# Kernel tuning notes

Hardware: AMD Instinct MI355X
Metric: run time of the kernel (lower is better)

Reference implementation:

```python
import jax, jax.numpy as jnp
import numpy as np

B, N, NPOINT, NSAMPLE = 16, 4096, 1024, 32
RADIUS = 0.4
MLP = [64, 64, 128]
IN_CH = 6
EPS = 1e-5


def setup_inputs() -> dict:
    key = jax.random.key(0)
    ks = jax.random.split(key, 2 + 2 * len(MLP))
    inp = {
        "xyz": jax.random.normal(ks[0], (B, 3, N), jnp.float32),
        "points": jax.random.normal(ks[1], (B, 3, N), jnp.float32),
    }
    c_in = IN_CH
    for i, c_out in enumerate(MLP):
        inp[f"W{i}"] = jax.random.normal(ks[2 + 2 * i], (c_out, c_in), jnp.float32) / np.sqrt(c_in).astype(np.float32)
        inp[f"b{i}"] = jnp.zeros((c_out,), jnp.float32)
        inp[f"g{i}"] = jnp.ones((c_out,), jnp.float32)
        inp[f"beta{i}"] = jnp.zeros((c_out,), jnp.float32)
        c_in = c_out
    return inp


def _gather(points, idx):
    # points: [B, N, C], idx: [B, ...] int -> [B, ..., C]
    Bv = points.shape[0]
    flat = idx.reshape(Bv, -1)
    out = jnp.take_along_axis(points, flat[..., None], axis=1)
    return out.reshape(idx.shape + (points.shape[-1],))


def _fps(xyz, npoint):
    # xyz: [B, N, 3] -> centroid indices [B, npoint]
    Bv, Nv, _ = xyz.shape
    bidx = jnp.arange(Bv)

    def step(carry, _):
        dist, far = carry
        cen = xyz[bidx, far][:, None, :]                 # [B,1,3]
        d = jnp.sum((xyz - cen) ** 2, axis=-1)           # [B,N]
        dist = jnp.minimum(dist, d)
        return (dist, jnp.argmax(dist, axis=-1)), far

    init = (jnp.full((Bv, Nv), 1e10, xyz.dtype), jnp.zeros((Bv,), jnp.int32))
    _, cents = jax.lax.scan(step, init, None, length=npoint)
    return jnp.transpose(cents)                          # [B, npoint]


def _square_distance(src, dst):
    # src [B,S,3], dst [B,N,3] -> [B,S,N]
    return (jnp.sum(src ** 2, -1)[:, :, None]
            + jnp.sum(dst ** 2, -1)[:, None, :]
            - 2.0 * jnp.einsum('bsc,bnc->bsn', src, dst))


def _ball_query(radius, nsample, xyz, new_xyz):
    Nv = xyz.shape[1]
    sqr = _square_distance(new_xyz, xyz)                 # [B,S,N]
    arange = jnp.arange(Nv, dtype=jnp.int32)[None, None, :]
    idx = jnp.where(sqr > radius ** 2, Nv, arange)       # invalid -> sentinel N
    idx = jnp.sort(idx, axis=-1)[:, :, :nsample]         # [B,S,K]
    first = idx[:, :, :1]
    return jnp.where(idx == Nv, first, idx)


def reference(xyz, points, W0, b0, g0, beta0, W1, b1, g1, beta1, W2, b2, g2, beta2):
    xyz_t = jnp.transpose(xyz, (0, 2, 1))                # [B,N,3]
    pts_t = jnp.transpose(points, (0, 2, 1))             # [B,N,D]

    fps_idx = _fps(xyz_t, NPOINT)                        # [B,S]
    new_xyz = _gather(xyz_t, fps_idx)                    # [B,S,3]
    idx = _ball_query(RADIUS, NSAMPLE, xyz_t, new_xyz)   # [B,S,K]

    g_xyz = _gather(xyz_t, idx) - new_xyz[:, :, None, :] # [B,S,K,3]
    g_pts = _gather(pts_t, idx)                          # [B,S,K,D]
    feats = jnp.concatenate([g_xyz, g_pts], axis=-1)     # [B,S,K,C]

    for W, b, g, be in ((W0, b0, g0, beta0), (W1, b1, g1, beta1), (W2, b2, g2, beta2)):
        feats = jnp.einsum('bskc,oc->bsko', feats, W) + b
        mean = feats.mean(axis=(0, 1, 2))                # BN train mode stats
        var = feats.var(axis=(0, 1, 2))
        feats = g * (feats - mean) * jax.lax.rsqrt(var + EPS) + be
        feats = jax.nn.relu(feats)

    out = feats.max(axis=2)                              # max over nsample -> [B,S,C]
    return jnp.transpose(new_xyz, (0, 2, 1)), jnp.transpose(out, (0, 2, 1))
```

## Files before the change

### kernel.cpp

```cpp
#include <hip/hip_runtime.h>
#include <hip/hip_bf16.h>

#define B_ 16
#define N_ 4096
#define S_ 1024
#define K_ 32
#define R_ (B_*S_*K_)
#define NBLK_ (R_/64)

typedef unsigned short u16;
typedef __attribute__((ext_vector_type(8))) short bf16x8;
typedef __attribute__((ext_vector_type(4))) float f32x4;

__device__ __forceinline__ u16 f2bf(float f) {
    __hip_bfloat16 h = __float2bfloat16(f);
    return __builtin_bit_cast(u16, h);
}
__device__ __forceinline__ float bf2f(u16 u) {
    unsigned x = ((unsigned)u) << 16;
    return __builtin_bit_cast(float, x);
}

template <int CTRL>
__device__ __forceinline__ double dpp_max_f64(double v) {
    unsigned long long b = (unsigned long long)__double_as_longlong(v);
    int lo = (int)(unsigned)b;
    int hi = (int)(unsigned)(b >> 32);
    int olo = __builtin_amdgcn_update_dpp(lo, lo, CTRL, 0xF, 0xF, false);
    int ohi = __builtin_amdgcn_update_dpp(hi, hi, CTRL, 0xF, 0xF, false);
    double o = __longlong_as_double(
        (long long)(((unsigned long long)(unsigned)ohi << 32) | (unsigned)olo));
    return fmax(v, o);
}

__device__ __forceinline__ double packd(double d, int idx) {
    unsigned long long b = (unsigned long long)__double_as_longlong(d);
    b = (b & ~0xFFFull) | (unsigned)idx;
    return __longlong_as_double((long long)b);
}

__global__ __launch_bounds__(512, 1) void fps_kernel(const float* __restrict__ xyz,
                                                     float* __restrict__ out0) {
    const int b = blockIdx.x;
    const int tid = threadIdx.x;
    const int lane = tid & 63, wid = tid >> 6;
    __shared__ double4 cd[N_];
    __shared__ double candd[2][8];
    const float* xb = xyz + (size_t)b * 3 * N_;

    double x64[8], y64[8], z64[8], q64[8], dist[8];
#pragma unroll
    for (int j = 0; j < 8; ++j) {
        int i = tid + j * 512;
        float x = xb[i], y = xb[N_ + i], z = xb[2 * N_ + i];
        double dx = (double)x, dy = (double)y, dz = (double)z;
        double q = dx * dx + dy * dy + dz * dz;
        double4 v; v.x = -2.0 * dx; v.y = -2.0 * dy; v.z = -2.0 * dz; v.w = q + 1.0;
        cd[i] = v;
        x64[j] = dx; y64[j] = dy; z64[j] = dz; q64[j] = q;
        dist[j] = 1e30;
    }
    __syncthreads();

    int far = 0;
    int f0 = 0, f1 = 0;
    for (int s = 0; s < 1023; ++s) {
        double4 C = cd[far];
        f0 = (tid == s) ? far : f0;
        f1 = (tid + 512 == s) ? far : f1;
#pragma unroll
        for (int j = 0; j < 8; ++j) {
            double d = fma(C.x, x64[j], fma(C.y, y64[j], fma(C.z, z64[j], q64[j] + C.w)));
            dist[j] = fmin(dist[j], packd(d, tid | (j << 9)));
        }
        double k = fmax(fmax(fmax(dist[0], dist[1]), fmax(dist[2], dist[3])),
                        fmax(fmax(dist[4], dist[5]), fmax(dist[6], dist[7])));
        k = dpp_max_f64<0x111>(k);
        k = dpp_max_f64<0x112>(k);
        k = dpp_max_f64<0x114>(k);
        k = dpp_max_f64<0x118>(k);
        k = dpp_max_f64<0x142>(k);
        k = dpp_max_f64<0x143>(k);
        int buf = s & 1;
        if (lane == 63) candd[buf][wid] = k;
        __syncthreads();
        double k2 = candd[buf][lane & 7];
        k2 = dpp_max_f64<0xB1>(k2);
        k2 = dpp_max_f64<0x4E>(k2);
        k2 = dpp_max_f64<0x124>(k2);
        unsigned lo = (unsigned)(unsigned long long)__double_as_longlong(k2);
        far = (int)(__builtin_amdgcn_readfirstlane(lo) & 0xFFFu);
    }
    if (tid == 511) f1 = far;
    {
        double4 c0 = cd[f0];
        out0[(size_t)b * 3072 + tid]        = (float)(-0.5 * c0.x);
        out0[(size_t)b * 3072 + 1024 + tid] = (float)(-0.5 * c0.y);
        out0[(size_t)b * 3072 + 2048 + tid] = (float)(-0.5 * c0.z);
        double4 c1 = cd[f1];
        out0[(size_t)b * 3072 + 512 + tid]        = (float)(-0.5 * c1.x);
        out0[(size_t)b * 3072 + 1024 + 512 + tid] = (float)(-0.5 * c1.y);
        out0[(size_t)b * 3072 + 2048 + 512 + tid] = (float)(-0.5 * c1.z);
    }
}

__global__ __launch_bounds__(256) void prep_kernel(const float* __restrict__ xyz,
                                                   const float* __restrict__ W1,
                                                   const float* __restrict__ W2,
                                                   u16* __restrict__ W1bf,
                                                   u16* __restrict__ W2bf,
                                                   double4* __restrict__ xyzq) {
    int t = blockIdx.x * 256 + threadIdx.x;
    if (t < 4096) W1bf[t] = f2bf(W1[t]);
    if (t < 8192) W2bf[t] = f2bf(W2[t]);
    int b = t >> 12, i = t & 4095;
    const float* xb = xyz + (size_t)b * 3 * N_;
    double x = (double)xb[i], y = (double)xb[N_ + i], z = (double)xb[2 * N_ + i];
    double4 v; v.x = x; v.y = y; v.z = z; v.w = x * x + y * y + z * z;
    xyzq[t] = v;
}

__global__ __launch_bounds__(256) void ballq_gather(
        const double4* __restrict__ xyzq, const float* __restrict__ out0,
        const float* __restrict__ xyz, const float* __restrict__ pts,
        int* __restrict__ idxbuf, float* __restrict__ F,
        float* __restrict__ part0) {
    __shared__ int idxs[4][32];
    __shared__ float Ftile[128][6];
    __shared__ float red[8][27];
    int wid = threadIdx.x >> 6, lane = threadIdx.x & 63;
    int m = blockIdx.x * 4 + wid;
    int b = m >> 10, s = m & 1023;
    const double4* pb = xyzq + (size_t)b * N_;
    double cx = (double)out0[b * 3072 + s];
    double cy = (double)out0[b * 3072 + 1024 + s];
    double cz = (double)out0[b * 3072 + 2048 + s];
    double c2 = cx * cx + cy * cy + cz * cz;
    const double rr = 0.4 * 0.4;
    int* ob = idxbuf + (size_t)m * K_;
    int cnt = 0, first = -1;
    for (int ch = 0; ch < N_ / 64; ++ch) {
        int i = ch * 64 + lane;
        double4 p = pb[i];
        double dot = cx * p.x + cy * p.y + cz * p.z;
        double sqr = (c2 + p.w) - 2.0 * dot;
        bool in = !(sqr > rr);
        unsigned long long mask = __ballot(in);
        if (in) {
            int pos = cnt + __popcll(mask & ((1ull << lane) - 1ull));
            if (pos < K_) { ob[pos] = i; idxs[wid][pos] = i; }
        }
        if (cnt == 0 && mask) first = ch * 64 + (__ffsll((long long)mask) - 1);
        cnt += __popcll(mask);
        if (cnt >= K_) break;
    }
    if (cnt < K_ && lane >= cnt && lane < K_) { ob[lane] = first; idxs[wid][lane] = first; }
    __syncthreads();
    if (lane < 32) {
        int i = idxs[wid][lane];
        int rl = wid * 32 + lane;
        long rw = (long)m * 32 + lane;
        float cxf = out0[b * 3072 + s], cyf = out0[b * 3072 + 1024 + s], czf = out0[b * 3072 + 2048 + s];
        const float* xb = xyz + (size_t)b * 3 * N_;
        const float* pp = pts + (size_t)b * 3 * N_;
        float f0v = xb[i] - cxf, f1v = xb[N_ + i] - cyf, f2v = xb[2 * N_ + i] - czf;
        float f3v = pp[i], f4v = pp[N_ + i], f5v = pp[2 * N_ + i];
        Ftile[rl][0] = f0v; Ftile[rl][1] = f1v; Ftile[rl][2] = f2v;
        Ftile[rl][3] = f3v; Ftile[rl][4] = f4v; Ftile[rl][5] = f5v;
        float* Fg = F + rw * 6;
        Fg[0] = f0v; Fg[1] = f1v; Fg[2] = f2v; Fg[3] = f3v; Fg[4] = f4v; Fg[5] = f5v;
    }
    __syncthreads();
    int t = threadIdx.x;
    if (t < 216) {
        const int c1t[27] = {0,1,2,3,4,5, 0,0,0,0,0,0, 1,1,1,1,1, 2,2,2,2, 3,3,3, 4,4, 5};
        const int c2t[27] = {0,1,2,3,4,5, 0,1,2,3,4,5, 1,2,3,4,5, 2,3,4,5, 3,4,5, 4,5, 5};
        int st = t % 27, g = t / 27;
        float acc = 0.f;
        if (st < 6) {
            for (int r = g * 16; r < g * 16 + 16; ++r) acc += Ftile[r][st];
        } else {
            int a = c1t[st], c = c2t[st];
            for (int r = g * 16; r < g * 16 + 16; ++r) acc += Ftile[r][a] * Ftile[r][c];
        }
        red[g][st] = acc;
    }
    __syncthreads();
    if (t < 27) {
        float a = 0.f;
#pragma unroll
        for (int g = 0; g < 8; ++g) a += red[g][t];
        part0[(size_t)blockIdx.x * 27 + t] = a;
    }
}

__global__ __launch_bounds__(256) void reduce27(const float* __restrict__ part0,
                                                double* __restrict__ G) {
    int st = blockIdx.x;
    int tid = threadIdx.x;
    double s = 0.0;
    for (int i = tid; i < 4096; i += 256) s += (double)part0[(size_t)i * 27 + st];
    __shared__ double ss[256];
    ss[tid] = s;
    __syncthreads();
    for (int m = 128; m > 0; m >>= 1) {
        if (tid < m) ss[tid] += ss[tid + m];
        __syncthreads();
    }
    if (tid == 0) G[st] = ss[0];
}

__global__ __launch_bounds__(64) void stats0_final(const double* __restrict__ G,
                                                   const float* __restrict__ W0,
                                                   const float* __restrict__ b0,
                                                   const float* __restrict__ g0,
                                                   const float* __restrict__ beta0,
                                                   float* __restrict__ scale0,
                                                   float* __restrict__ shift0) {
    int o = threadIdx.x;
    double w[6], mvec[6];
#pragma unroll
    for (int c = 0; c < 6; ++c) { w[c] = (double)W0[o * 6 + c]; mvec[c] = G[c]; }
    double dot = 0.0;
#pragma unroll
    for (int c = 0; c < 6; ++c) dot += w[c] * mvec[c];
    const double Rd = (double)R_;
    double bb = (double)b0[o];
    double mu = dot / Rd + bb;
    double quad = 0.0;
    int k = 6;
#pragma unroll
    for (int a = 0; a < 6; ++a)
#pragma unroll
        for (int c = a; c < 6; ++c) {
            double g = G[k++];
            quad += (a == c) ? w[a] * w[c] * g : 2.0 * w[a] * w[c] * g;
        }
    double ey2 = (quad + 2.0 * bb * dot) / Rd + bb * bb;
    double var = ey2 - mu * mu;
    double sc = (double)g0[o] / sqrt(var + 1e-5);
    scale0[o] = (float)sc;
    shift0[o] = (float)((double)beta0[o] - mu * sc);
}

__global__ __launch_bounds__(256) void reduce_stats(const float2* __restrict__ part,
                                                    int nblk, int C,
                                                    const float* __restrict__ g,
                                                    const float* __restrict__ beta,
                                                    float* __restrict__ scale,
                                                    float* __restrict__ shift) {
    int o = blockIdx.x;
    int tid = threadIdx.x;
    double s = 0.0, q = 0.0;
    for (int i = tid; i < nblk; i += 256) {
        float2 v = part[(size_t)i * C + o];
        s += (double)v.x; q += (double)v.y;
    }
    __shared__ double ss[256], qq[256];
    ss[tid] = s; qq[tid] = q;
    __syncthreads();
    for (int m = 128; m > 0; m >>= 1) {
        if (tid < m) { ss[tid] += ss[tid + m]; qq[tid] += qq[tid + m]; }
        __syncthreads();
    }
    if (tid == 0) {
        const double Rd = (double)R_;
        double mean = ss[0] / Rd;
        double var = qq[0] / Rd - mean * mean;
        double sc = (double)g[o] / sqrt(var + 1e-5);
        scale[o] = (float)sc;
        shift[o] = (float)((double)beta[o] - mean * sc);
    }
}

__global__ __launch_bounds__(256) void layer1_mfma(
        const float* __restrict__ F, const float* __restrict__ W0,
        const float* __restrict__ b0, const float* __restrict__ scale0,
        const float* __restrict__ shift0, const u16* __restrict__ W1bf,
        const float* __restrict__ b1, u16* __restrict__ Y1bf,
        float2* __restrict__ part) {
    __shared__ float Fs[64][6];
    __shared__ float W0s[384];
    __shared__ float b0s[64], sc0[64], sh0[64];
    __shared__ u16 Xs[64][72];
    __shared__ float ssum[16][64];
    __shared__ float ssq[16][64];
    int tid = threadIdx.x;
    long rowbase = (long)blockIdx.x * 64;
    for (int t = tid; t < 384; t += 256) { Fs[t / 6][t % 6] = F[rowbase * 6 + t]; W0s[t] = W0[t]; }
    if (tid < 64) { b0s[tid] = b0[tid]; sc0[tid] = scale0[tid]; sh0[tid] = shift0[tid]; }
    __syncthreads();
    {
        int o = tid & 63, rg = tid >> 6;
        float w[6];
#pragma unroll
        for (int c = 0; c < 6; ++c) w[c] = W0s[o * 6 + c];
        float sc = sc0[o], sh = sh0[o], bb = b0s[o];
#pragma unroll
        for (int rr = 0; rr < 16; ++rr) {
            int rl = rg * 16 + rr;
            float y = bb;
#pragma unroll
            for (int c = 0; c < 6; ++c) y += Fs[rl][c] * w[c];
            Xs[rl][o] = f2bf(fmaxf(sc * y + sh, 0.f));
        }
    }
    __syncthreads();
    int l = tid & 63, w = tid >> 6;
    int ar = l & 15, kg = l >> 4;
    bf16x8 a0 = *(const bf16x8*)&Xs[w * 16 + ar][kg * 8];
    bf16x8 a1 = *(const bf16x8*)&Xs[w * 16 + ar][32 + kg * 8];
    f32x4 acc[4];
#pragma unroll
    for (int t4 = 0; t4 < 4; ++t4) acc[t4] = (f32x4){0.f, 0.f, 0.f, 0.f};
#pragma unroll
    for (int t4 = 0; t4 < 4; ++t4) {
        const u16* wp = &W1bf[(t4 * 16 + ar) * 64 + kg * 8];
        bf16x8 bfr0 = *(const bf16x8*)wp;
        bf16x8 bfr1 = *(const bf16x8*)(wp + 32);
        acc[t4] = __builtin_amdgcn_mfma_f32_16x16x32_bf16(a0, bfr0, acc[t4], 0, 0, 0);
        acc[t4] = __builtin_amdgcn_mfma_f32_16x16x32_bf16(a1, bfr1, acc[t4], 0, 0, 0);
    }
#pragma unroll
    for (int t4 = 0; t4 < 4; ++t4) {
        int col = t4 * 16 + ar;
        float bb = b1[col];
        float s = 0.f, q = 0.f;
#pragma unroll
        for (int r = 0; r < 4; ++r) {
            float y = acc[t4][r] + bb;
            int row = w * 16 + kg * 4 + r;
            Y1bf[(rowbase + row) * 64 + col] = f2bf(y);
            s += y; q += y * y;
        }
        ssum[w * 4 + kg][col] = s;
        ssq[w * 4 + kg][col] = q;
    }
    __syncthreads();
    if (tid < 64) {
        float s = 0.f, q = 0.f;
#pragma unroll
        for (int i = 0; i < 16; ++i) { s += ssum[i][tid]; q += ssq[i][tid]; }
        part[(size_t)blockIdx.x * 64 + tid] = make_float2(s, q);
    }
}

__global__ __launch_bounds__(256) void layer2_mfma(
        const u16* __restrict__ Y1bf, const float* __restrict__ scale1,
        const float* __restrict__ shift1, const u16* __restrict__ W2bf,
        const float* __restrict__ b2, float* __restrict__ gmax,
        float* __restrict__ gmin, float2* __restrict__ part) {
    __shared__ u16 Xs[64][72];
    __shared__ float sc1s[64], sh1s[64];
    __shared__ float mxs[16][128], mns[16][128];
    __shared__ float ssum[16][128], ssq[16][128];
    int tid = threadIdx.x;
    long rowbase = (long)blockIdx.x * 64;
    if (tid < 64) { sc1s[tid] = scale1[tid]; sh1s[tid] = shift1[tid]; }
    __syncthreads();
    {
        int r = tid >> 2, seg = (tid & 3) * 16;
        const u16* yp = &Y1bf[(rowbase + r) * 64 + seg];
        bf16x8 v0 = *(const bf16x8*)yp;
        bf16x8 v1 = *(const bf16x8*)(yp + 8);
#pragma unroll
        for (int j = 0; j < 8; ++j) {
            float x0 = fmaxf(sc1s[seg + j] * bf2f((u16)v0[j]) + sh1s[seg + j], 0.f);
            float x1 = fmaxf(sc1s[seg + 8 + j] * bf2f((u16)v1[j]) + sh1s[seg + 8 + j], 0.f);
            Xs[r][seg + j] = f2bf(x0);
            Xs[r][seg + 8 + j] = f2bf(x1);
        }
    }
    __syncthreads();
    int l = tid & 63, w = tid >> 6;
    int ar = l & 15, kg = l >> 4;
    bf16x8 a0 = *(const bf16x8*)&Xs[w * 16 + ar][kg * 8];
    bf16x8 a1 = *(const bf16x8*)&Xs[w * 16 + ar][32 + kg * 8];
    f32x4 acc[8];
#pragma unroll
    for (int t8 = 0; t8 < 8; ++t8) acc[t8] = (f32x4){0.f, 0.f, 0.f, 0.f};
#pragma unroll
    for (int t8 = 0; t8 < 8; ++t8) {
        const u16* wp = &W2bf[(t8 * 16 + ar) * 64 + kg * 8];
        bf16x8 bfr0 = *(const bf16x8*)wp;
        bf16x8 bfr1 = *(const bf16x8*)(wp + 32);
        acc[t8] = __builtin_amdgcn_mfma_f32_16x16x32_bf16(a0, bfr0, acc[t8], 0, 0, 0);
        acc[t8] = __builtin_amdgcn_mfma_f32_16x16x32_bf16(a1, bfr1, acc[t8], 0, 0, 0);
    }
#pragma unroll
    for (int t8 = 0; t8 < 8; ++t8) {
        int col = t8 * 16 + ar;
        float bb = b2[col];
        float y0 = acc[t8][0] + bb, y1 = acc[t8][1] + bb;
        float y2 = acc[t8][2] + bb, y3 = acc[t8][3] + bb;
        ssum[w * 4 + kg][col] = y0 + y1 + y2 + y3;
        ssq[w * 4 + kg][col] = y0 * y0 + y1 * y1 + y2 * y2 + y3 * y3;
        mxs[w * 4 + kg][col] = fmaxf(fmaxf(y0, y1), fmaxf(y2, y3));
        mns[w * 4 + kg][col] = fminf(fminf(y0, y1), fminf(y2, y3));
    }
    __syncthreads();
    if (tid < 128) {
        int col = tid;
        float s = 0.f, q = 0.f;
        float m0 = -3.0e38f, m1 = -3.0e38f, n0 = 3.0e38f, n1 = 3.0e38f;
#pragma unroll
        for (int i = 0; i < 8; ++i) {
            s += ssum[i][col]; q += ssq[i][col];
            m0 = fmaxf(m0, mxs[i][col]); n0 = fminf(n0, mns[i][col]);
        }
#pragma unroll
        for (int i = 8; i < 16; ++i) {
            s += ssum[i][col]; q += ssq[i][col];
            m1 = fmaxf(m1, mxs[i][col]); n1 = fminf(n1, mns[i][col]);
        }
        part[(size_t)blockIdx.x * 128 + col] = make_float2(s, q);
        gmax[((size_t)blockIdx.x * 2 + 0) * 128 + col] = m0;
        gmax[((size_t)blockIdx.x * 2 + 1) * 128 + col] = m1;
        gmin[((size_t)blockIdx.x * 2 + 0) * 128 + col] = n0;
        gmin[((size_t)blockIdx.x * 2 + 1) * 128 + col] = n1;
    }
}

__global__ __launch_bounds__(256) void final_kernel(const float* __restrict__ gmax,
                                                    const float* __restrict__ gmin,
                                                    const float* __restrict__ scale2,
                                                    const float* __restrict__ shift2,
                                                    float* __restrict__ out1) {
    int b = blockIdx.x, st = blockIdx.y, ot = blockIdx.z;
    __shared__ float tile[32][33];
    int tid = threadIdx.x;
    for (int e = tid; e < 1024; e += 256) {
        int sl = e >> 5, ol = e & 31;
        int s = st * 32 + sl, o = ot * 32 + ol;
        size_t m = (size_t)b * 1024 + s;
        float sc = scale2[o];
        float v = (sc >= 0.f) ? gmax[m * 128 + o] : gmin[m * 128 + o];
        tile[sl][ol] = fmaxf(sc * v + shift2[o], 0.f);
    }
    __syncthreads();
    for (int e = tid; e < 1024; e += 256) {
        int ol = e >> 5, sl = e & 31;
        int s = st * 32 + sl, o = ot * 32 + ol;
        out1[(size_t)b * 131072 + (size_t)o * 1024 + s] = tile[sl][ol];
    }
}

extern "C" void kernel_launch(void* const* d_in, const int* in_sizes, int n_in,
                              void* d_out, int out_size, void* d_ws, size_t ws_size,
                              hipStream_t stream) {
    const float* xyz   = (const float*)d_in[0];
    const float* pts   = (const float*)d_in[1];
    const float* W0    = (const float*)d_in[2];
    const float* b0    = (const float*)d_in[3];
    const float* g0    = (const float*)d_in[4];
    const float* beta0 = (const float*)d_in[5];
    const float* W1    = (const float*)d_in[6];
    const float* b1    = (const float*)d_in[7];
    const float* g1    = (const float*)d_in[8];
    const float* beta1 = (const float*)d_in[9];
    const float* W2    = (const float*)d_in[10];
    const float* b2    = (const float*)d_in[11];
    const float* g2    = (const float*)d_in[12];
    const float* beta2 = (const float*)d_in[13];

    float* out0 = (float*)d_out;
    float* out1 = (float*)d_out + 49152;

    char* w = (char*)d_ws;
    size_t off = 0;
    double4* xyzq = (double4*)(w + off);  off += (size_t)B_ * N_ * 32;
    int*    idxbuf = (int*)(w + off);    off += (size_t)R_ * 4;
    float*  F      = (float*)(w + off);  off += (size_t)R_ * 6 * 4;
    u16*    Y1bf   = (u16*)(w + off);    off += (size_t)R_ * 64 * 2;
    float*  gmax   = (float*)(w + off);  off += (size_t)B_ * S_ * 128 * 4;
    float*  gmin   = (float*)(w + off);  off += (size_t)B_ * S_ * 128 * 4;
    float2* part   = (float2*)(w + off); off += (size_t)NBLK_ * 128 * 2 * 4;
    float*  part0  = (float*)(w + off);  off += (size_t)4096 * 27 * 4;
    double* G27    = (double*)(w + off); off += 32 * 8;
    u16*    W1bf   = (u16*)(w + off);    off += 4096 * 2;
    u16*    W2bf   = (u16*)(w + off);    off += 8192 * 2;
    float*  ss     = (float*)(w + off);  off += 512 * 4;
    float* scale0 = ss,       *shift0 = ss + 64;
    float* scale1 = ss + 128, *shift1 = ss + 192;
    float* scale2 = ss + 256, *shift2 = ss + 384;

    prep_kernel<<<256, 256, 0, stream>>>(xyz, W1, W2, W1bf, W2bf, xyzq);
    fps_kernel<<<B_, 512, 0, stream>>>(xyz, out0);
    ballq_gather<<<(B_ * S_) / 4, 256, 0, stream>>>(xyzq, out0, xyz, pts, idxbuf, F, part0);
    reduce27<<<27, 256, 0, stream>>>(part0, G27);
    stats0_final<<<1, 64, 0, stream>>>(G27, W0, b0, g0, beta0, scale0, shift0);
    layer1_mfma<<<NBLK_, 256, 0, stream>>>(F, W0, b0, scale0, shift0, W1bf, b1, Y1bf, part);
    reduce_stats<<<64, 256, 0, stream>>>(part, NBLK_, 64, g1, beta1, scale1, shift1);
    layer2_mfma<<<NBLK_, 256, 0, stream>>>(Y1bf, scale1, shift1, W2bf, b2, gmax, gmin, part);
    reduce_stats<<<128, 256, 0, stream>>>(part, NBLK_, 128, g2, beta2, scale2, shift2);
    final_kernel<<<dim3(B_, 32, 4), 256, 0, stream>>>(gmax, gmin, scale2, shift2, out1);
}
```

Measured before the change: 813.7 us.

## Double MLP block tiles to 128 rows and share one LDS reduction buffer

The layer1 and layer2 MFMA kernels now handle 128 rows per block with 512 threads, which halves the number of per-block partial-stat records for reduce_stats. Layer2 replaces its four separate LDS reduction arrays with one buffer that is reused in sequence for sum, sum of squares, max and min, so shared memory stays small at the larger tile. The price is more barriers and recomputing bias-added values. The gather in ballq_gather also spreads the xyz and points loads across all 64 lanes instead of 32.

```diff
diff --git a/kernel.cpp b/kernel.cpp
--- a/kernel.cpp
+++ b/kernel.cpp
@@ -6,7 +6,7 @@
 #define S_ 1024
 #define K_ 32
 #define R_ (B_*S_*K_)
-#define NBLK_ (R_/64)
+#define NB1_ (R_/128)
 
 typedef unsigned short u16;
 typedef __attribute__((ext_vector_type(8))) short bf16x8;
@@ -156,19 +156,25 @@
     }
     if (cnt < K_ && lane >= cnt && lane < K_) { ob[lane] = first; idxs[wid][lane] = first; }
     __syncthreads();
-    if (lane < 32) {
-        int i = idxs[wid][lane];
-        int rl = wid * 32 + lane;
-        long rw = (long)m * 32 + lane;
-        float cxf = out0[b * 3072 + s], cyf = out0[b * 3072 + 1024 + s], czf = out0[b * 3072 + 2048 + s];
-        const float* xb = xyz + (size_t)b * 3 * N_;
-        const float* pp = pts + (size_t)b * 3 * N_;
-        float f0v = xb[i] - cxf, f1v = xb[N_ + i] - cyf, f2v = xb[2 * N_ + i] - czf;
-        float f3v = pp[i], f4v = pp[N_ + i], f5v = pp[2 * N_ + i];
-        Ftile[rl][0] = f0v; Ftile[rl][1] = f1v; Ftile[rl][2] = f2v;
-        Ftile[rl][3] = f3v; Ftile[rl][4] = f4v; Ftile[rl][5] = f5v;
+    {
+        int l2 = lane & 31;
+        int i = idxs[wid][l2];
+        int rl = wid * 32 + l2;
+        long rw = (long)m * 32 + l2;
         float* Fg = F + rw * 6;
-        Fg[0] = f0v; Fg[1] = f1v; Fg[2] = f2v; Fg[3] = f3v; Fg[4] = f4v; Fg[5] = f5v;
+        if (lane < 32) {
+            float cxf = out0[b * 3072 + s], cyf = out0[b * 3072 + 1024 + s],
+                  czf = out0[b * 3072 + 2048 + s];
+            const float* xb = xyz + (size_t)b * 3 * N_;
+            float f0v = xb[i] - cxf, f1v = xb[N_ + i] - cyf, f2v = xb[2 * N_ + i] - czf;
+            Ftile[rl][0] = f0v; Ftile[rl][1] = f1v; Ftile[rl][2] = f2v;
+            Fg[0] = f0v; Fg[1] = f1v; Fg[2] = f2v;
+        } else {
+            const float* pp = pts + (size_t)b * 3 * N_;
+            float f3v = pp[i], f4v = pp[N_ + i], f5v = pp[2 * N_ + i];
+            Ftile[rl][3] = f3v; Ftile[rl][4] = f4v; Ftile[rl][5] = f5v;
+            Fg[3] = f3v; Fg[4] = f4v; Fg[5] = f5v;
+        }
     }
     __syncthreads();
     int t = threadIdx.x;
@@ -273,21 +279,22 @@
     }
 }
 
-__global__ __launch_bounds__(256) void layer1_mfma(
+__global__ __launch_bounds__(512) void layer1_mfma(
         const float* __restrict__ F, const float* __restrict__ W0,
         const float* __restrict__ b0, const float* __restrict__ scale0,
         const float* __restrict__ shift0, const u16* __restrict__ W1bf,
         const float* __restrict__ b1, u16* __restrict__ Y1bf,
         float2* __restrict__ part) {
-    __shared__ float Fs[64][6];
+    __shared__ float Fs[128][6];
     __shared__ float W0s[384];
     __shared__ float b0s[64], sc0[64], sh0[64];
-    __shared__ u16 Xs[64][72];
-    __shared__ float ssum[16][64];
-    __shared__ float ssq[16][64];
+    __shared__ u16 Xs[128][72];
+    __shared__ float ssum[32][64];
+    __shared__ float ssq[32][64];
     int tid = threadIdx.x;
-    long rowbase = (long)blockIdx.x * 64;
-    for (int t = tid; t < 384; t += 256) { Fs[t / 6][t % 6] = F[rowbase * 6 + t]; W0s[t] = W0[t]; }
+    long rowbase = (long)blockIdx.x * 128;
+    for (int t = tid; t < 768; t += 512) Fs[t / 6][t % 6] = F[rowbase * 6 + t];
+    if (tid < 384) W0s[tid] = W0[tid];
     if (tid < 64) { b0s[tid] = b0[tid]; sc0[tid] = scale0[tid]; sh0[tid] = shift0[tid]; }
     __syncthreads();
     {
@@ -340,22 +347,21 @@
     if (tid < 64) {
         float s = 0.f, q = 0.f;
 #pragma unroll
-        for (int i = 0; i < 16; ++i) { s += ssum[i][tid]; q += ssq[i][tid]; }
+        for (int i = 0; i < 32; ++i) { s += ssum[i][tid]; q += ssq[i][tid]; }
         part[(size_t)blockIdx.x * 64 + tid] = make_float2(s, q);
     }
 }
 
-__global__ __launch_bounds__(256) void layer2_mfma(
+__global__ __launch_bounds__(512) void layer2_mfma(
         const u16* __restrict__ Y1bf, const float* __restrict__ scale1,
         const float* __restrict__ shift1, const u16* __restrict__ W2bf,
         const float* __restrict__ b2, float* __restrict__ gmax,
         float* __restrict__ gmin, float2* __restrict__ part) {
-    __shared__ u16 Xs[64][72];
+    __shared__ u16 Xs[128][72];
     __shared__ float sc1s[64], sh1s[64];
-    __shared__ float mxs[16][128], mns[16][128];
-    __shared__ float ssum[16][128], ssq[16][128];
+    __shared__ float red[32][128];
     int tid = threadIdx.x;
-    long rowbase = (long)blockIdx.x * 64;
+    long rowbase = (long)blockIdx.x * 128;
     if (tid < 64) { sc1s[tid] = scale1[tid]; sh1s[tid] = shift1[tid]; }
     __syncthreads();
     {
@@ -387,37 +393,58 @@
         acc[t8] = __builtin_amdgcn_mfma_f32_16x16x32_bf16(a0, bfr0, acc[t8], 0, 0, 0);
         acc[t8] = __builtin_amdgcn_mfma_f32_16x16x32_bf16(a1, bfr1, acc[t8], 0, 0, 0);
     }
+    float ybias[8];
+#pragma unroll
+    for (int t8 = 0; t8 < 8; ++t8) ybias[t8] = b2[t8 * 16 + ar];
 #pragma unroll
     for (int t8 = 0; t8 < 8; ++t8) {
-        int col = t8 * 16 + ar;
-        float bb = b2[col];
-        float y0 = acc[t8][0] + bb, y1 = acc[t8][1] + bb;
-        float y2 = acc[t8][2] + bb, y3 = acc[t8][3] + bb;
-        ssum[w * 4 + kg][col] = y0 + y1 + y2 + y3;
-        ssq[w * 4 + kg][col] = y0 * y0 + y1 * y1 + y2 * y2 + y3 * y3;
-        mxs[w * 4 + kg][col] = fmaxf(fmaxf(y0, y1), fmaxf(y2, y3));
-        mns[w * 4 + kg][col] = fminf(fminf(y0, y1), fminf(y2, y3));
+        float y0 = acc[t8][0] + ybias[t8], y1 = acc[t8][1] + ybias[t8];
+        float y2 = acc[t8][2] + ybias[t8], y3 = acc[t8][3] + ybias[t8];
+        red[w * 4 + kg][t8 * 16 + ar] = y0 + y1 + y2 + y3;
+    }
+    __syncthreads();
+    float psum = 0.f;
+    if (tid < 128) { for (int i = 0; i < 32; ++i) psum += red[i][tid]; }
+    __syncthreads();
+#pragma unroll
+    for (int t8 = 0; t8 < 8; ++t8) {
+        float y0 = acc[t8][0] + ybias[t8], y1 = acc[t8][1] + ybias[t8];
+        float y2 = acc[t8][2] + ybias[t8], y3 = acc[t8][3] + ybias[t8];
+        red[w * 4 + kg][t8 * 16 + ar] = y0 * y0 + y1 * y1 + y2 * y2 + y3 * y3;
     }
     __syncthreads();
     if (tid < 128) {
-        int col = tid;
-        float s = 0.f, q = 0.f;
-        float m0 = -3.0e38f, m1 = -3.0e38f, n0 = 3.0e38f, n1 = 3.0e38f;
-#pragma unroll
-        for (int i = 0; i < 8; ++i) {
-            s += ssum[i][col]; q += ssq[i][col];
-            m0 = fmaxf(m0, mxs[i][col]); n0 = fminf(n0, mns[i][col]);
-        }
-#pragma unroll
-        for (int i = 8; i < 16; ++i) {
-            s += ssum[i][col]; q += ssq[i][col];
-            m1 = fmaxf(m1, mxs[i][col]); n1 = fminf(n1, mns[i][col]);
-        }
-        part[(size_t)blockIdx.x * 128 + col] = make_float2(s, q);
-        gmax[((size_t)blockIdx.x * 2 + 0) * 128 + col] = m0;
-        gmax[((size_t)blockIdx.x * 2 + 1) * 128 + col] = m1;
-        gmin[((size_t)blockIdx.x * 2 + 0) * 128 + col] = n0;
-        gmin[((size_t)blockIdx.x * 2 + 1) * 128 + col] = n1;
+        float psq = 0.f;
+        for (int i = 0; i < 32; ++i) psq += red[i][tid];
+        part[(size_t)blockIdx.x * 128 + tid] = make_float2(psum, psq);
+    }
+    __syncthreads();
+#pragma unroll
+    for (int t8 = 0; t8 < 8; ++t8) {
+        float y0 = acc[t8][0] + ybias[t8], y1 = acc[t8][1] + ybias[t8];
+        float y2 = acc[t8][2] + ybias[t8], y3 = acc[t8][3] + ybias[t8];
+        red[w * 4 + kg][t8 * 16 + ar] = fmaxf(fmaxf(y0, y1), fmaxf(y2, y3));
+    }
+    __syncthreads();
+    {
+        int gsel = tid >> 7, col = tid & 127;
+        float mv = -3.0e38f;
+        for (int rp = gsel * 8; rp < gsel * 8 + 8; ++rp) mv = fmaxf(mv, red[rp][col]);
+        gmax[((size_t)blockIdx.x * 4 + gsel) * 128 + col] = mv;
+    }
+    __syncthreads();
+#pragma unroll
+    for (int t8 = 0; t8 < 8; ++t8) {
+        float y0 = acc[t8][0] + ybias[t8], y1 = acc[t8][1] + ybias[t8];
+        float y2 = acc[t8][2] + ybias[t8], y3 = acc[t8][3] + ybias[t8];
+        red[w * 4 + kg][t8 * 16 + ar] = fminf(fminf(y0, y1), fminf(y2, y3));
+    }
+    __syncthreads();
+    {
+        int gsel = tid >> 7, col = tid & 127;
+        float mv = 3.0e38f;
+        for (int rp = gsel * 8; rp < gsel * 8 + 8; ++rp) mv = fminf(mv, red[rp][col]);
+        gmin[((size_t)blockIdx.x * 4 + gsel) * 128 + col] = mv;
     }
 }
 
@@ -474,7 +501,7 @@
     u16*    Y1bf   = (u16*)(w + off);    off += (size_t)R_ * 64 * 2;
     float*  gmax   = (float*)(w + off);  off += (size_t)B_ * S_ * 128 * 4;
     float*  gmin   = (float*)(w + off);  off += (size_t)B_ * S_ * 128 * 4;
-    float2* part   = (float2*)(w + off); off += (size_t)NBLK_ * 128 * 2 * 4;
+    float2* part   = (float2*)(w + off); off += (size_t)NB1_ * 128 * 2 * 4;
     float*  part0  = (float*)(w + off);  off += (size_t)4096 * 27 * 4;
     double* G27    = (double*)(w + off); off += 32 * 8;
     u16*    W1bf   = (u16*)(w + off);    off += 4096 * 2;
@@ -489,9 +516,9 @@
     ballq_gather<<<(B_ * S_) / 4, 256, 0, stream>>>(xyzq, out0, xyz, pts, idxbuf, F, part0);
     reduce27<<<27, 256, 0, stream>>>(part0, G27);
     stats0_final<<<1, 64, 0, stream>>>(G27, W0, b0, g0, beta0, scale0, shift0);
-    layer1_mfma<<<NBLK_, 256, 0, stream>>>(F, W0, b0, scale0, shift0, W1bf, b1, Y1bf, part);
-    reduce_stats<<<64, 256, 0, stream>>>(part, NBLK_, 64, g1, beta1, scale1, shift1);
-    layer2_mfma<<<NBLK_, 256, 0, stream>>>(Y1bf, scale1, shift1, W2bf, b2, gmax, gmin, part);
-    reduce_stats<<<128, 256, 0, stream>>>(part, NBLK_, 128, g2, beta2, scale2, shift2);
+    layer1_mfma<<<NB1_, 512, 0, stream>>>(F, W0, b0, scale0, shift0, W1bf, b1, Y1bf, part);
+    reduce_stats<<<64, 256, 0, stream>>>(part, NB1_, 64, g1, beta1, scale1, shift1);
+    layer2_mfma<<<NB1_, 512, 0, stream>>>(Y1bf, scale1, shift1, W2bf, b2, gmax, gmin, part);
+    reduce_stats<<<128, 256, 0, stream>>>(part, NB1_, 128, g2, beta2, scale2, shift2);
     final_kernel<<<dim3(B_, 32, 4), 256, 0, stream>>>(gmax, gmin, scale2, shift2, out1);
 }
```

Result: faster. 794.1 us (-2.4%).
